# Kernel optimization log

Measured on AMD Instinct MI355X. Metric: run time of the kernel, lower is better.

## Reference

```python
import jax, jax.numpy as jnp
import numpy as np

N, S, D = 4, 2048, 1024
H, HD = 16, 64  # heads, head_dim = patch_size // heads
SCALE = 1.0 / np.float32(np.sqrt(D))  # module divides by sqrt(patch_size), not sqrt(head_dim)


def setup_inputs() -> dict:
    key = jax.random.key(0)
    ks = jax.random.split(key, 8)
    return {
        "values": jax.random.normal(ks[0], (N, S, D), dtype=jnp.float32),
        "keys": jax.random.normal(ks[1], (N, S, D), dtype=jnp.float32),
        "query": jax.random.normal(ks[2], (N, S, D), dtype=jnp.float32),
        "Wv": jax.random.normal(ks[3], (HD, HD), dtype=jnp.float32) / np.float32(np.sqrt(HD)),
        "Wk": jax.random.normal(ks[4], (HD, HD), dtype=jnp.float32) / np.float32(np.sqrt(HD)),
        "Wq": jax.random.normal(ks[5], (HD, HD), dtype=jnp.float32) / np.float32(np.sqrt(HD)),
        "Wo": jax.random.normal(ks[6], (D, D), dtype=jnp.float32) / np.float32(np.sqrt(D)),
        "bo": jnp.zeros((D,), dtype=jnp.float32),
    }


def reference(values, keys, query, Wv, Wk, Wq, Wo, bo):
    n, ql = query.shape[0], query.shape[1]
    # reshape to heads, then per-head shared linear projections (torch Linear: x @ W.T)
    v = jnp.einsum('nlhd,ed->nlhe', values.reshape(n, -1, H, HD), Wv)
    k = jnp.einsum('nkhd,ed->nkhe', keys.reshape(n, -1, H, HD), Wk)
    q = jnp.einsum('nqhd,ed->nqhe', query.reshape(n, -1, H, HD), Wq)
    energy = jnp.einsum('nqhd,nkhd->nhqk', q, k)  # [N,H,Sq,Sk]
    attn = jax.nn.softmax(energy * SCALE, axis=3)
    out = jnp.einsum('nhql,nlhd->nqhd', attn, v).reshape(n, ql, H * HD)
    return out @ Wo.T + bo
```

## Files before the change

kernel.cpp:

```cpp
#include <hip/hip_runtime.h>
#include <stdint.h>

typedef _Float16 f16;
typedef f16 half2_t __attribute__((ext_vector_type(2)));
typedef f16 half4_t __attribute__((ext_vector_type(4)));
typedef f16 half8_t __attribute__((ext_vector_type(8)));
typedef __fp16 fp16x2_t __attribute__((ext_vector_type(2)));
typedef float f32x4 __attribute__((ext_vector_type(4)));

#define N_ 4
#define S_ 2048
#define D_ 1024
#define H_ 16
#define HD_ 64
#define LOG2E 1.44269504088896340736f
#define SCALE_ 0.03125f

typedef __attribute__((address_space(1))) void gvoid;
typedef __attribute__((address_space(3))) void lvoid;

__device__ __forceinline__ void load_lds16(const void* g, void* l) {
  __builtin_amdgcn_global_load_lds((gvoid*)(uintptr_t)g, (lvoid*)l, 16, 0, 0);
}

__device__ __forceinline__ f32x4 mfma16(half4_t a, half4_t b, f32x4 c) {
  return __builtin_amdgcn_mfma_f32_16x16x16f16(a, b, c, 0, 0, 0);
}
__device__ __forceinline__ f32x4 mfma32(half8_t a, half8_t b, f32x4 c) {
  return __builtin_amdgcn_mfma_f32_16x16x32_f16(a, b, c, 0, 0, 0);
}

__device__ __forceinline__ half2_t pack_f16(float a, float b) {
  fp16x2_t t = __builtin_amdgcn_cvt_pkrtz(a, b);
  return __builtin_bit_cast(half2_t, t);
}

#define LO4(v) __builtin_shufflevector(v, v, 0, 1, 2, 3)
#define HI4(v) __builtin_shufflevector(v, v, 4, 5, 6, 7)

__global__ void wprep(const float* __restrict__ Wv, const float* __restrict__ Wo,
                      const float* __restrict__ Wq, const float* __restrict__ Wk,
                      f16* __restrict__ Wbig, float* __restrict__ Mq) {
  int b = blockIdx.x;
  if (b < 1024) {
    int j = b;
#pragma unroll
    for (int c = 0; c < 4; ++c) {
      int i = c * 256 + threadIdx.x;
      int h = i >> 6, dd = i & 63;
      const float* wo = Wo + (size_t)j * 1024 + h * 64;
      float acc = 0.f;
#pragma unroll 8
      for (int e = 0; e < 64; ++e) acc += Wv[e * 64 + dd] * wo[e];
      Wbig[(size_t)j * 1024 + i] = (f16)acc;
    }
  } else {
    int tid = (b - 1024) * 256 + threadIdx.x;
    int d = tid >> 6, e = tid & 63;
    float acc = 0.f;
#pragma unroll 8
    for (int r = 0; r < 64; ++r) acc += Wq[r * 64 + d] * Wk[r * 64 + e];
    Mq[d * 64 + e] = acc * (SCALE_ * LOG2E);
  }
}

__global__ __launch_bounds__(256) void prep2(const float* __restrict__ Q,
                                             const float* __restrict__ K,
                                             const float* __restrict__ V,
                                             const float* __restrict__ Mq,
                                             f16* __restrict__ q16, f16* __restrict__ k16,
                                             f16* __restrict__ v16) {
  __shared__ char smem[16384];
  int b = blockIdx.x;
  if (b < 512) {
    float* mql = (float*)smem;
#pragma unroll
    for (int c = 0; c < 16; ++c) mql[c * 256 + threadIdx.x] = Mq[c * 256 + threadIdx.x];
    __syncthreads();
    int n = b >> 7, sblk = b & 127;
    int L = threadIdx.x & 63, w = threadIdx.x >> 6;
    int lq = L & 15, hh = w * 4 + (L >> 4);
    int s = sblk * 16 + lq;
    const float* qrow = Q + ((size_t)(n * S_ + s)) * D_ + hh * HD_;
    f32x4 acc4[16];
#pragma unroll
    for (int i = 0; i < 16; ++i) acc4[i] = (f32x4){0.f, 0.f, 0.f, 0.f};
    for (int d4 = 0; d4 < 16; ++d4) {
      f32x4 qv = *(const f32x4*)(qrow + d4 * 4);
#pragma unroll
      for (int dj = 0; dj < 4; ++dj) {
        const f32x4* mrow = (const f32x4*)(mql + (d4 * 4 + dj) * 64);
        float qs = qv[dj];
#pragma unroll
        for (int i = 0; i < 16; ++i) acc4[i] += mrow[i] * qs;
      }
    }
    size_t cbase = ((size_t)((n * 16 + hh) * 128 + sblk)) * 2;
#pragma unroll
    for (int dp = 0; dp < 2; ++dp) {
#pragma unroll
      for (int qd = 0; qd < 4; ++qd) {
        half8_t hv;
        f32x4 a0 = acc4[dp * 8 + qd * 2], a1 = acc4[dp * 8 + qd * 2 + 1];
#pragma unroll
        for (int j = 0; j < 4; ++j) { hv[j] = (f16)a0[j]; hv[4 + j] = (f16)a1[j]; }
        *(half8_t*)(q16 + (cbase + dp) * 512 + (qd * 16 + lq) * 8) = hv;
      }
    }
    const float* krow = K + ((size_t)(n * S_ + s)) * D_ + hh * HD_;
    f32x4 kr[16];
#pragma unroll
    for (int i = 0; i < 16; ++i) kr[i] = *(const f32x4*)(krow + i * 4);
#pragma unroll
    for (int dp = 0; dp < 2; ++dp) {
#pragma unroll
      for (int qd = 0; qd < 4; ++qd) {
        half8_t hv;
        f32x4 a0 = kr[dp * 8 + qd * 2], a1 = kr[dp * 8 + qd * 2 + 1];
#pragma unroll
        for (int j = 0; j < 4; ++j) { hv[j] = (f16)a0[j]; hv[4 + j] = (f16)a1[j]; }
        *(half8_t*)(k16 + (cbase + dp) * 512 + (qd * 16 + lq) * 8) = hv;
      }
    }
  } else {
    f16* lv = (f16*)smem;
    int b2 = b - 512;
    int n = b2 >> 10, hh = (b2 >> 6) & 15, sb = b2 & 63;
    int t = threadIdx.x;
    {
      int r = t >> 3, ic = t & 7;
      const float* src = V + ((size_t)(n * S_ + sb * 32 + r)) * D_ + hh * HD_ + ic * 8;
      f32x4 a = *(const f32x4*)src;
      f32x4 b3 = *(const f32x4*)(src + 4);
      half8_t hv;
#pragma unroll
      for (int j = 0; j < 4; ++j) { hv[j] = (f16)a[j]; hv[4 + j] = (f16)b3[j]; }
      *(half8_t*)(lv + r * 64 + ic * 8) = hv;
    }
    __syncthreads();
    {
      int mt = t >> 6, L = t & 63;
      int quad = L >> 4, ld = L & 15;
      half8_t o;
#pragma unroll
      for (int j = 0; j < 4; ++j) {
        o[j]     = lv[(quad * 4 + j) * 64 + mt * 16 + ld];
        o[4 + j] = lv[(quad * 4 + j + 16) * 64 + mt * 16 + ld];
      }
      *(half8_t*)(v16 + (((size_t)(n * 16 + hh) * 64 + sb) * 4 + mt) * 512 + L * 8) = o;
    }
  }
}

__global__ __launch_bounds__(256, 4) void flash(const f16* __restrict__ q16,
                                                const f16* __restrict__ k16,
                                                const f16* __restrict__ v16,
                                                f16* __restrict__ att) {
  __shared__ char lds[32768];
  int nh = blockIdx.x;
  int qt2 = blockIdx.y;
  int L = threadIdx.x & 63, w = threadIdx.x >> 6;
  int lq = L & 15, quad = L >> 4;

  const half8_t* qg = (const half8_t*)q16;
  half8_t qB[2][2];
#pragma unroll
  for (int j = 0; j < 2; ++j) {
    size_t qc = ((size_t)(nh * 128 + qt2 * 8 + w * 2 + j)) * 2;
    qB[j][0] = qg[qc * 64 + L];
    qB[j][1] = qg[(qc + 1) * 64 + L];
  }

  f32x4 accO[2][4];
#pragma unroll
  for (int j = 0; j < 2; ++j)
#pragma unroll
    for (int i = 0; i < 4; ++i) accO[j][i] = (f32x4){0.f, 0.f, 0.f, 0.f};
  f32x4 lvec[2] = {(f32x4){0.f, 0.f, 0.f, 0.f}, (f32x4){0.f, 0.f, 0.f, 0.f}};

  const char* kg = (const char*)k16 + (size_t)nh * 262144 + w * 4096 + L * 16;
  const char* vg = (const char*)v16 + (size_t)nh * 262144 + w * 4096 + L * 16;
  char* lk = lds + w * 4096;
  char* lv = lds + 16384 + w * 4096;

#pragma unroll
  for (int c = 0; c < 4; ++c) load_lds16(kg + c * 1024, lk + c * 1024);
#pragma unroll
  for (int c = 0; c < 4; ++c) load_lds16(vg + c * 1024, lv + c * 1024);
  __syncthreads();

  for (int it = 0; it < 16; ++it) {
    half4_t pc[2][8];
#pragma unroll
    for (int mt = 0; mt < 8; ++mt) {
      half8_t k0 = *(const half8_t*)(lds + (mt * 2 + 0) * 1024 + L * 16);
      half8_t k1 = *(const half8_t*)(lds + (mt * 2 + 1) * 1024 + L * 16);
#pragma unroll
      for (int j = 0; j < 2; ++j) {
        f32x4 a = (f32x4){0.f, 0.f, 0.f, 0.f};
        a = mfma32(k0, qB[j][0], a);
        a = mfma32(k1, qB[j][1], a);
        f32x4 p;
#pragma unroll
        for (int r = 0; r < 4; ++r) p[r] = __builtin_amdgcn_exp2f(a[r]);
        lvec[j] += p;
        half2_t c01 = pack_f16(p[0], p[1]);
        half2_t c23 = pack_f16(p[2], p[3]);
        pc[j][mt] = __builtin_shufflevector(c01, c23, 0, 1, 2, 3);
      }
    }
    __syncthreads();
    if (it < 15) {
#pragma unroll
      for (int c = 0; c < 4; ++c) load_lds16(kg + 16384 + c * 1024, lk + c * 1024);
      kg += 16384;
    }

#pragma unroll
    for (int mt2 = 0; mt2 < 4; ++mt2) {
      f32x4 a0 = accO[0][mt2], a1 = accO[1][mt2];
#pragma unroll
      for (int kp = 0; kp < 4; ++kp) {
        half8_t vf = *(const half8_t*)(lds + 16384 + (kp * 4 + mt2) * 1024 + L * 16);
        half4_t vlo = LO4(vf), vhi = HI4(vf);
        a0 = mfma16(vlo, pc[0][2 * kp], a0);
        a0 = mfma16(vhi, pc[0][2 * kp + 1], a0);
        a1 = mfma16(vlo, pc[1][2 * kp], a1);
        a1 = mfma16(vhi, pc[1][2 * kp + 1], a1);
      }
      accO[0][mt2] = a0; accO[1][mt2] = a1;
    }
    __syncthreads();
    if (it < 15) {
#pragma unroll
      for (int c = 0; c < 4; ++c) load_lds16(vg + 16384 + c * 1024, lv + c * 1024);
      vg += 16384;
    }
  }

  int n = nh >> 4, h = nh & 15;
#pragma unroll
  for (int j = 0; j < 2; ++j) {
    float l = lvec[j][0] + lvec[j][1] + lvec[j][2] + lvec[j][3];
    l += __shfl_xor(l, 16, 64);
    l += __shfl_xor(l, 32, 64);
    float inv_l = 1.0f / l;
    int s = qt2 * 128 + (w * 2 + j) * 16 + lq;
    f16* orow = att + ((size_t)(n * S_ + s)) * D_ + h * HD_;
#pragma unroll
    for (int mt2 = 0; mt2 < 4; ++mt2) {
      half4_t o;
#pragma unroll
      for (int r = 0; r < 4; ++r) o[r] = (f16)(accO[j][mt2][r] * inv_l);
      *(half4_t*)(orow + mt2 * 16 + quad * 4) = o;
    }
  }
}

__global__ __launch_bounds__(256) void ogemm(const f16* __restrict__ A, const f16* __restrict__ Bm,
                                             const float* __restrict__ bias, float* __restrict__ C) {
  __shared__ char lds[16384];
  int bm = blockIdx.x, bn = blockIdx.y;
  int L = threadIdx.x & 63, w = threadIdx.x >> 6;
  int wm = w >> 1, wn = w & 1;
  int lq = L & 15, quad = L >> 4;
  int lr = L >> 2, lc = L & 3;
  int src_c = lc ^ (lr & 3);
  f32x4 acc[16];
#pragma unroll
  for (int i = 0; i < 16; ++i) acc[i] = (f32x4){0.f, 0.f, 0.f, 0.f};

  const f16* ga0 = A + ((size_t)(bm * 128 + (w * 2) * 16 + lr)) * 1024 + src_c * 8;
  const f16* gb0 = Bm + ((size_t)(bn * 128 + (w * 2) * 16 + lr)) * 1024 + src_c * 8;

#pragma unroll
  for (int c = 0; c < 2; ++c) {
    load_lds16(ga0 + (size_t)c * 16 * 1024, lds + (w * 2 + c) * 1024);
    load_lds16(gb0 + (size_t)c * 16 * 1024, lds + 8192 + (w * 2 + c) * 1024);
  }
  __syncthreads();

  for (int kt = 0; kt < 32; ++kt) {
    half8_t af[4], bf[4];
#pragma unroll
    for (int t = 0; t < 4; ++t) {
      int ch = quad ^ (lq & 3);
      af[t] = *(const half8_t*)(lds + (wm * 64 + t * 16 + lq) * 64 + ch * 16);
      bf[t] = *(const half8_t*)(lds + 8192 + (wn * 64 + t * 16 + lq) * 64 + ch * 16);
    }
    __syncthreads();
    if (kt < 31) {
#pragma unroll
      for (int c = 0; c < 2; ++c) {
        load_lds16(ga0 + (kt + 1) * 32 + (size_t)c * 16 * 1024, lds + (w * 2 + c) * 1024);
        load_lds16(gb0 + (kt + 1) * 32 + (size_t)c * 16 * 1024, lds + 8192 + (w * 2 + c) * 1024);
      }
    }
#pragma unroll
    for (int mt = 0; mt < 4; ++mt)
#pragma unroll
      for (int nt = 0; nt < 4; ++nt)
        acc[mt * 4 + nt] =
            __builtin_amdgcn_mfma_f32_16x16x32_f16(af[mt], bf[nt], acc[mt * 4 + nt], 0, 0, 0);
    __syncthreads();
  }

#pragma unroll
  for (int nt = 0; nt < 4; ++nt) {
    int col = bn * 128 + wn * 64 + nt * 16 + lq;
    float bv = bias[col];
#pragma unroll
    for (int mt = 0; mt < 4; ++mt) {
#pragma unroll
      for (int r = 0; r < 4; ++r) {
        int row = bm * 128 + wm * 64 + mt * 16 + quad * 4 + r;
        C[(size_t)row * 1024 + col] = acc[mt * 4 + nt][r] + bv;
      }
    }
  }
}

extern "C" void kernel_launch(void* const* d_in, const int* in_sizes, int n_in,
                              void* d_out, int out_size, void* d_ws, size_t ws_size,
                              hipStream_t stream) {
  const float* V  = (const float*)d_in[0];
  const float* K  = (const float*)d_in[1];
  const float* Q  = (const float*)d_in[2];
  const float* Wv = (const float*)d_in[3];
  const float* Wk = (const float*)d_in[4];
  const float* Wq = (const float*)d_in[5];
  const float* Wo = (const float*)d_in[6];
  const float* bo = (const float*)d_in[7];
  float* out = (float*)d_out;

  char* ws = (char*)d_ws;
  float* Mq  = (float*)(ws);
  f16* Wbig  = (f16*)(ws + (1ull << 20));
  f16* q16   = (f16*)(ws + (3ull << 20));
  f16* k16   = (f16*)(ws + (19ull << 20));
  f16* v16   = (f16*)(ws + (35ull << 20));
  f16* att   = (f16*)(ws + (51ull << 20));

  wprep<<<1040, 256, 0, stream>>>(Wv, Wo, Wq, Wk, Wbig, Mq);
  prep2<<<4608, 256, 0, stream>>>(Q, K, V, Mq, q16, k16, v16);
  flash<<<dim3(64, 16), 256, 0, stream>>>(q16, k16, v16, att);
  ogemm<<<dim3(64, 8), 256, 0, stream>>>(att, Wbig, bo, out);
}
```

Before: 294.7 us.

## Double-buffer K/V tiles in flash and A/B tiles in output GEMM

Both the flash attention kernel and the output-projection GEMM move from single-buffered LDS staging to two buffers, prefetching tile it+2 while computing tile it. In flash, the QK/exp and PV MFMA stages are also interleaved in groups of four, so probabilities are consumed right away and fewer registers stay live. This halves the barriers per iteration and aims to hide global-to-LDS latency. In exchange LDS use doubles (64KB for flash, 32KB for ogemm) and the flash occupancy hint drops from 4 to 2 blocks per CU.

```diff
diff --git a/kernel.cpp b/kernel.cpp
--- a/kernel.cpp
+++ b/kernel.cpp
@@ -152,11 +152,11 @@
   }
 }
 
-__global__ __launch_bounds__(256, 4) void flash(const f16* __restrict__ q16,
+__global__ __launch_bounds__(256, 2) void flash(const f16* __restrict__ q16,
                                                 const f16* __restrict__ k16,
                                                 const f16* __restrict__ v16,
                                                 f16* __restrict__ att) {
-  __shared__ char lds[32768];
+  __shared__ char lds[65536];
   int nh = blockIdx.x;
   int qt2 = blockIdx.y;
   int L = threadIdx.x & 63, w = threadIdx.x >> 6;
@@ -180,61 +180,62 @@
 
   const char* kg = (const char*)k16 + (size_t)nh * 262144 + w * 4096 + L * 16;
   const char* vg = (const char*)v16 + (size_t)nh * 262144 + w * 4096 + L * 16;
-  char* lk = lds + w * 4096;
-  char* lv = lds + 16384 + w * 4096;
-
-#pragma unroll
-  for (int c = 0; c < 4; ++c) load_lds16(kg + c * 1024, lk + c * 1024);
-#pragma unroll
-  for (int c = 0; c < 4; ++c) load_lds16(vg + c * 1024, lv + c * 1024);
+
+#pragma unroll
+  for (int t = 0; t < 2; ++t)
+#pragma unroll
+    for (int c = 0; c < 4; ++c) {
+      load_lds16(kg + t * 16384 + c * 1024, lds + t * 16384 + w * 4096 + c * 1024);
+      load_lds16(vg + t * 16384 + c * 1024, lds + 32768 + t * 16384 + w * 4096 + c * 1024);
+    }
   __syncthreads();
 
   for (int it = 0; it < 16; ++it) {
-    half4_t pc[2][8];
-#pragma unroll
-    for (int mt = 0; mt < 8; ++mt) {
-      half8_t k0 = *(const half8_t*)(lds + (mt * 2 + 0) * 1024 + L * 16);
-      half8_t k1 = *(const half8_t*)(lds + (mt * 2 + 1) * 1024 + L * 16);
-#pragma unroll
-      for (int j = 0; j < 2; ++j) {
-        f32x4 a = (f32x4){0.f, 0.f, 0.f, 0.f};
-        a = mfma32(k0, qB[j][0], a);
-        a = mfma32(k1, qB[j][1], a);
-        f32x4 p;
-#pragma unroll
-        for (int r = 0; r < 4; ++r) p[r] = __builtin_amdgcn_exp2f(a[r]);
-        lvec[j] += p;
-        half2_t c01 = pack_f16(p[0], p[1]);
-        half2_t c23 = pack_f16(p[2], p[3]);
-        pc[j][mt] = __builtin_shufflevector(c01, c23, 0, 1, 2, 3);
+    const char* kb = lds + (it & 1) * 16384;
+    const char* vb = lds + 32768 + (it & 1) * 16384;
+#pragma unroll
+    for (int g = 0; g < 4; ++g) {
+      half4_t pcg[2][2];
+#pragma unroll
+      for (int u = 0; u < 2; ++u) {
+        int mt = 2 * g + u;
+        half8_t k0 = *(const half8_t*)(kb + (mt * 2 + 0) * 1024 + L * 16);
+        half8_t k1 = *(const half8_t*)(kb + (mt * 2 + 1) * 1024 + L * 16);
+#pragma unroll
+        for (int j = 0; j < 2; ++j) {
+          f32x4 a = (f32x4){0.f, 0.f, 0.f, 0.f};
+          a = mfma32(k0, qB[j][0], a);
+          a = mfma32(k1, qB[j][1], a);
+          f32x4 p;
+#pragma unroll
+          for (int r = 0; r < 4; ++r) p[r] = __builtin_amdgcn_exp2f(a[r]);
+          lvec[j] += p;
+          half2_t c01 = pack_f16(p[0], p[1]);
+          half2_t c23 = pack_f16(p[2], p[3]);
+          pcg[j][u] = __builtin_shufflevector(c01, c23, 0, 1, 2, 3);
+        }
+      }
+#pragma unroll
+      for (int mt2 = 0; mt2 < 4; ++mt2) {
+        half8_t vf = *(const half8_t*)(vb + (g * 4 + mt2) * 1024 + L * 16);
+        half4_t vlo = LO4(vf), vhi = HI4(vf);
+        f32x4 a0 = accO[0][mt2], a1 = accO[1][mt2];
+        a0 = mfma16(vlo, pcg[0][0], a0);
+        a0 = mfma16(vhi, pcg[0][1], a0);
+        a1 = mfma16(vlo, pcg[1][0], a1);
+        a1 = mfma16(vhi, pcg[1][1], a1);
+        accO[0][mt2] = a0; accO[1][mt2] = a1;
       }
     }
     __syncthreads();
-    if (it < 15) {
-#pragma unroll
-      for (int c = 0; c < 4; ++c) load_lds16(kg + 16384 + c * 1024, lk + c * 1024);
-      kg += 16384;
-    }
-
-#pragma unroll
-    for (int mt2 = 0; mt2 < 4; ++mt2) {
-      f32x4 a0 = accO[0][mt2], a1 = accO[1][mt2];
-#pragma unroll
-      for (int kp = 0; kp < 4; ++kp) {
-        half8_t vf = *(const half8_t*)(lds + 16384 + (kp * 4 + mt2) * 1024 + L * 16);
-        half4_t vlo = LO4(vf), vhi = HI4(vf);
-        a0 = mfma16(vlo, pc[0][2 * kp], a0);
-        a0 = mfma16(vhi, pc[0][2 * kp + 1], a0);
-        a1 = mfma16(vlo, pc[1][2 * kp], a1);
-        a1 = mfma16(vhi, pc[1][2 * kp + 1], a1);
-      }
-      accO[0][mt2] = a0; accO[1][mt2] = a1;
-    }
-    __syncthreads();
-    if (it < 15) {
-#pragma unroll
-      for (int c = 0; c < 4; ++c) load_lds16(vg + 16384 + c * 1024, lv + c * 1024);
-      vg += 16384;
+    if (it + 2 < 16) {
+      char* dk = lds + (it & 1) * 16384 + w * 4096;
+      char* dv = lds + 32768 + (it & 1) * 16384 + w * 4096;
+#pragma unroll
+      for (int c = 0; c < 4; ++c) {
+        load_lds16(kg + (size_t)(it + 2) * 16384 + c * 1024, dk + c * 1024);
+        load_lds16(vg + (size_t)(it + 2) * 16384 + c * 1024, dv + c * 1024);
+      }
     }
   }
 
@@ -257,9 +258,9 @@
   }
 }
 
-__global__ __launch_bounds__(256) void ogemm(const f16* __restrict__ A, const f16* __restrict__ Bm,
-                                             const float* __restrict__ bias, float* __restrict__ C) {
-  __shared__ char lds[16384];
+__global__ __launch_bounds__(256, 2) void ogemm(const f16* __restrict__ A, const f16* __restrict__ Bm,
+                                                const float* __restrict__ bias, float* __restrict__ C) {
+  __shared__ char lds[32768];
   int bm = blockIdx.x, bn = blockIdx.y;
   int L = threadIdx.x & 63, w = threadIdx.x >> 6;
   int wm = w >> 1, wn = w & 1;
@@ -274,27 +275,22 @@
   const f16* gb0 = Bm + ((size_t)(bn * 128 + (w * 2) * 16 + lr)) * 1024 + src_c * 8;
 
 #pragma unroll
-  for (int c = 0; c < 2; ++c) {
-    load_lds16(ga0 + (size_t)c * 16 * 1024, lds + (w * 2 + c) * 1024);
-    load_lds16(gb0 + (size_t)c * 16 * 1024, lds + 8192 + (w * 2 + c) * 1024);
-  }
+  for (int t = 0; t < 2; ++t)
+#pragma unroll
+    for (int c = 0; c < 2; ++c) {
+      load_lds16(ga0 + t * 32 + (size_t)c * 16 * 1024, lds + t * 16384 + (w * 2 + c) * 1024);
+      load_lds16(gb0 + t * 32 + (size_t)c * 16 * 1024, lds + t * 16384 + 8192 + (w * 2 + c) * 1024);
+    }
   __syncthreads();
 
   for (int kt = 0; kt < 32; ++kt) {
+    const char* base = lds + (kt & 1) * 16384;
     half8_t af[4], bf[4];
 #pragma unroll
     for (int t = 0; t < 4; ++t) {
       int ch = quad ^ (lq & 3);
-      af[t] = *(const half8_t*)(lds + (wm * 64 + t * 16 + lq) * 64 + ch * 16);
-      bf[t] = *(const half8_t*)(lds + 8192 + (wn * 64 + t * 16 + lq) * 64 + ch * 16);
-    }
-    __syncthreads();
-    if (kt < 31) {
-#pragma unroll
-      for (int c = 0; c < 2; ++c) {
-        load_lds16(ga0 + (kt + 1) * 32 + (size_t)c * 16 * 1024, lds + (w * 2 + c) * 1024);
-        load_lds16(gb0 + (kt + 1) * 32 + (size_t)c * 16 * 1024, lds + 8192 + (w * 2 + c) * 1024);
-      }
+      af[t] = *(const half8_t*)(base + (wm * 64 + t * 16 + lq) * 64 + ch * 16);
+      bf[t] = *(const half8_t*)(base + 8192 + (wn * 64 + t * 16 + lq) * 64 + ch * 16);
     }
 #pragma unroll
     for (int mt = 0; mt < 4; ++mt)
@@ -303,6 +299,14 @@
         acc[mt * 4 + nt] =
             __builtin_amdgcn_mfma_f32_16x16x32_f16(af[mt], bf[nt], acc[mt * 4 + nt], 0, 0, 0);
     __syncthreads();
+    if (kt + 2 < 32) {
+      char* dst = lds + (kt & 1) * 16384;
+#pragma unroll
+      for (int c = 0; c < 2; ++c) {
+        load_lds16(ga0 + (kt + 2) * 32 + (size_t)c * 16 * 1024, dst + (w * 2 + c) * 1024);
+        load_lds16(gb0 + (kt + 2) * 32 + (size_t)c * 16 * 1024, dst + 8192 + (w * 2 + c) * 1024);
+      }
+    }
   }
 
 #pragma unroll
```

After: 290.5 us. About the same (-1.4%).
